# Performance work log

Hardware: AMD Instinct MI355X
Metric: run time of the kernel (lower is better)

The kernel has to match this reference:

```python
import jax, jax.numpy as jnp
import numpy as np

K = 512           # num_embeddings
D = 256           # embedding_dim
GRID = (16, 32)   # SOM grid, prod == K
SIGMA = 2.0       # Gaussian neighborhood width (blur at step 0)
COMMITMENT_COST = 0.25
KOHONEN_COST = 1.0


def _make_blur_matrix():
    # Grid.init id->coord: coord[j] = (i // prod(shape[:j])) % shape[j]
    idx = np.arange(K)
    c0 = idx % GRID[0]
    c1 = (idx // GRID[0]) % GRID[1]
    coords = np.stack([c0, c1], axis=-1).astype(np.float32)  # [K, 2]
    dist = np.linalg.norm(coords[None, :, :] - coords[:, None, :], axis=-1)  # [K, K]
    return jnp.asarray(np.exp(-(dist ** 2) / (2.0 * SIGMA ** 2)), dtype=jnp.float32)


def setup_inputs() -> dict:
    key = jax.random.key(0)
    kx, kw = jax.random.split(key)
    x = jax.random.normal(kx, (64, 32, 32, D), dtype=jnp.float32)
    w = jax.random.normal(kw, (K, D), dtype=jnp.float32)
    bmat = _make_blur_matrix()  # [K, K] constant buffer
    return {"x": x, "w": w, "bmat": bmat}


def reference(x, w, bmat):
    sg = jax.lax.stop_gradient
    flat = x.reshape(-1, D)  # [N, D]

    # nearest-code search (no_grad in torch)
    fw = sg(flat)
    ww = sg(w)
    dists = (jnp.sum(fw ** 2, axis=1, keepdims=True)
             + jnp.sum(ww ** 2, axis=1)
             - 2.0 * fw @ ww.T)                       # [N, K]
    enc_idx = jnp.argmin(dists, axis=1)               # [N]
    encodings = jax.nn.one_hot(enc_idx, K, dtype=jnp.float32)  # [N, K]

    # embedding lookup (differentiable w.r.t. w)
    quant_flat = w[enc_idx]                           # [N, D]
    quantized = quant_flat.reshape(x.shape)

    # l2_batch(w, quantized.detach()) -> [N, K]
    qd = sg(quant_flat)
    diff = (jnp.sum(w ** 2, axis=1)[None, :]
            + jnp.sum(qd ** 2, axis=1, keepdims=True)
            - 2.0 * qd @ w.T)                         # [N, K]

    # blur-weighted kohonen loss: bmm(diff[N,1,K], bmat[idx][N,K,1]).mean()
    selected = bmat[enc_idx]                          # [N, K]
    kohonen_loss = jnp.mean(jnp.sum(diff * selected, axis=-1))

    avg_probs = jnp.mean(encodings, axis=0)
    perplexity = jnp.exp(-jnp.sum(avg_probs * jnp.log(avg_probs + 1e-10)))

    e_latent = jnp.mean((sg(quantized) - x) ** 2)
    q_latent = jnp.mean((quantized - sg(x)) ** 2)
    loss = q_latent + COMMITMENT_COST * e_latent + KOHONEN_COST * kohonen_loss

    quantized_st = x + sg(quantized - x)              # straight-through
    return loss, quantized_st, perplexity, enc_idx
```

## Files before the change

### kernel.cpp

```cpp
#include <hip/hip_runtime.h>
#include <hip/hip_bf16.h>
#include <hip/hip_fp16.h>
#include <math.h>

#define NPTS 65536
#define DIM  256
#define KC   512

#define BM    128
#define NBLK  (NPTS / BM)
#define XSTR  264
#define EPS   0.01f

#define QOFF  1
#define PIDX  16777217
#define EOFF  16777218

#define XSQ_OFF   532480
#define CAND_OFF  794624
#define WS_NEEDED (CAND_OFF + (size_t)8 * 65536 * 16)

typedef _Float16 h8    __attribute__((ext_vector_type(8)));
typedef float    f32x4 __attribute__((ext_vector_type(4)));

__device__ inline void cvt_split8(float4 a, float4 b, h8& hv, h8& lv) {
    float f[8] = {a.x, a.y, a.z, a.w, b.x, b.y, b.z, b.w};
    #pragma unroll
    for (int i = 0; i < 8; ++i) {
        _Float16 h = (_Float16)f[i];
        hv[i] = h;
        lv[i] = (_Float16)(f[i] - (float)h);
    }
}

__device__ inline void merge_top2(float& b1, int& i1, float& b2, int& i2,
                                  float ob1, int oi1, float ob2, int oi2) {
    bool ow = (ob1 < b1) || (ob1 == b1 && oi1 < i1);
    float lb = ow ? b1 : ob1; int li = ow ? i1 : oi1;
    if (ow) { b1 = ob1; i1 = oi1; }
    float c2 = b2; int ci = i2;
    if (ob2 < c2 || (ob2 == c2 && oi2 < ci)) { c2 = ob2; ci = oi2; }
    if (lb  < c2 || (lb  == c2 && li  < ci)) { c2 = lb;  ci = li;  }
    b2 = c2; i2 = ci;
}

__device__ inline float exact_dist(const float* __restrict__ xr,
                                   const float* __restrict__ w, int c, float wsqc) {
    const float* wr = w + (size_t)c * DIM;
    float d0 = 0.f, d1 = 0.f, d2 = 0.f, d3 = 0.f;
    #pragma unroll 4
    for (int d = 0; d < DIM; d += 4) {
        d0 = fmaf(xr[d + 0], wr[d + 0], d0);
        d1 = fmaf(xr[d + 1], wr[d + 1], d1);
        d2 = fmaf(xr[d + 2], wr[d + 2], d2);
        d3 = fmaf(xr[d + 3], wr[d + 3], d3);
    }
    return wsqc - 2.f * ((d0 + d1) + (d2 + d3));
}

__global__ __launch_bounds__(256) void som_wsq(const float* __restrict__ w,
                                               float* __restrict__ wsq,
                                               int* __restrict__ hist,
                                               double* __restrict__ mse_acc)
{
    int k = blockIdx.x * 256 + threadIdx.x;
    const float4* r = reinterpret_cast<const float4*>(w + (size_t)k * DIM);
    float s0 = 0.f, s1 = 0.f, s2 = 0.f, s3 = 0.f;
    #pragma unroll 8
    for (int q = 0; q < DIM / 4; ++q) {
        float4 v = r[q];
        s0 = fmaf(v.x, v.x, s0);
        s1 = fmaf(v.y, v.y, s1);
        s2 = fmaf(v.z, v.z, s2);
        s3 = fmaf(v.w, v.w, s3);
    }
    wsq[k] = (s0 + s1) + (s2 + s3);
    hist[k] = 0;
    if (k == 0) *mse_acc = 0.0;
}

__global__ __launch_bounds__(256) void som_conv(const float* __restrict__ w,
                                                _Float16* __restrict__ wfh,
                                                _Float16* __restrict__ wfl)
{
    const int tid = threadIdx.x;
    const int row = blockIdx.x * 8 + (tid >> 5);
    const int g   = tid & 31;
    const float4* r = reinterpret_cast<const float4*>(w + (size_t)row * DIM);
    float4 a = r[g * 2], b = r[g * 2 + 1];
    h8 hv, lv; cvt_split8(a, b, hv, lv);
    int dsl = g >> 2, kg = g & 3;
    int ctg = row >> 4, l15 = row & 15;
    size_t off = (((size_t)(ctg * 8 + dsl)) * 4 + kg) * 128 + l15 * 8;
    *reinterpret_cast<h8*>(wfh + off) = hv;
    *reinterpret_cast<h8*>(wfl + off) = lv;
}

__global__ __launch_bounds__(1024) void som_main2(const float* __restrict__ x,
                                                  const _Float16* __restrict__ wfh,
                                                  const _Float16* __restrict__ wfl,
                                                  const float* __restrict__ wsq,
                                                  float4* __restrict__ cand,
                                                  float* __restrict__ xsq_g)
{
    alignas(16) __shared__ _Float16 xh[BM * XSTR];
    alignas(16) __shared__ _Float16 xl[BM * XSTR];
    __shared__ float wsq_s[KC];

    const int tid  = threadIdx.x;
    const int lane = tid & 63;
    const int wid  = tid >> 6;
    const int l15  = lane & 15;
    const int kg   = lane >> 4;
    const int pgrp = wid & 1;
    const int cgrp = wid >> 1;
    const int ptBlock = blockIdx.x * BM;

    const float4* xg4 = reinterpret_cast<const float4*>(x);
    #pragma unroll
    for (int it = 0; it < 4; ++it) {
        int u = it * 1024 + tid, row = u >> 5, c8 = u & 31;
        float4 a = xg4[(size_t)(ptBlock + row) * 64 + c8 * 2];
        float4 b = xg4[(size_t)(ptBlock + row) * 64 + c8 * 2 + 1];
        h8 hv, lv; cvt_split8(a, b, hv, lv);
        *reinterpret_cast<h8*>(&xh[row * XSTR + c8 * 8]) = hv;
        *reinterpret_cast<h8*>(&xl[row * XSTR + c8 * 8]) = lv;
        float s = ((fmaf(a.x, a.x, a.y * a.y) + fmaf(a.z, a.z, a.w * a.w))
                 + (fmaf(b.x, b.x, b.y * b.y) + fmaf(b.z, b.z, b.w * b.w)));
        #pragma unroll
        for (int m = 1; m <= 16; m <<= 1) s += __shfl_xor(s, m, 64);
        if ((lane & 31) == 0) xsq_g[ptBlock + row] = s;
    }
    if (tid < KC) wsq_s[tid] = wsq[tid];
    __syncthreads();

    float sb[4], ss[4];
    int   ib[4], is2[4];
    #pragma unroll
    for (int ct = 0; ct < 4; ++ct) { sb[ct] = INFINITY; ss[ct] = INFINITY; ib[ct] = 0; is2[ct] = 0; }

    #pragma unroll 1
    for (int pass = 0; pass < 2; ++pass) {
        f32x4 acc[2][4];
        #pragma unroll
        for (int rt = 0; rt < 2; ++rt)
            #pragma unroll
            for (int ct = 0; ct < 4; ++ct)
                acc[rt][ct] = (f32x4){0.f, 0.f, 0.f, 0.f};

        #pragma unroll 1
        for (int dsl = 0; dsl < 8; ++dsl) {
            int boff0 = (pgrp * 64 + l15) * XSTR + dsl * 32 + kg * 8;
            h8 Bh[4];
            #pragma unroll
            for (int ct = 0; ct < 4; ++ct)
                Bh[ct] = *reinterpret_cast<const h8*>(&xh[boff0 + ct * 16 * XSTR]);
            h8 Ah[2], Al[2];
            #pragma unroll
            for (int rt = 0; rt < 2; ++rt) {
                int ctg = pass * 16 + cgrp * 2 + rt;
                size_t aoff = ((size_t)ctg * 8 + dsl) * 512 + kg * 128 + l15 * 8;
                Ah[rt] = *reinterpret_cast<const h8*>(wfh + aoff);
                Al[rt] = *reinterpret_cast<const h8*>(wfl + aoff);
            }
            #pragma unroll
            for (int rt = 0; rt < 2; ++rt)
                #pragma unroll
                for (int ct = 0; ct < 4; ++ct)
                    acc[rt][ct] = __builtin_amdgcn_mfma_f32_16x16x32_f16(Ah[rt], Bh[ct], acc[rt][ct], 0, 0, 0);
            #pragma unroll
            for (int rt = 0; rt < 2; ++rt)
                #pragma unroll
                for (int ct = 0; ct < 4; ++ct)
                    acc[rt][ct] = __builtin_amdgcn_mfma_f32_16x16x32_f16(Al[rt], Bh[ct], acc[rt][ct], 0, 0, 0);
            h8 Bl[4];
            #pragma unroll
            for (int ct = 0; ct < 4; ++ct)
                Bl[ct] = *reinterpret_cast<const h8*>(&xl[boff0 + ct * 16 * XSTR]);
            #pragma unroll
            for (int rt = 0; rt < 2; ++rt)
                #pragma unroll
                for (int ct = 0; ct < 4; ++ct)
                    acc[rt][ct] = __builtin_amdgcn_mfma_f32_16x16x32_f16(Ah[rt], Bl[ct], acc[rt][ct], 0, 0, 0);
        }

        #pragma unroll
        for (int rt = 0; rt < 2; ++rt) {
            #pragma unroll
            for (int r = 0; r < 4; ++r) {
                int cc = pass * 256 + cgrp * 32 + rt * 16 + kg * 4 + r;
                float wq = wsq_s[cc];
                #pragma unroll
                for (int ct = 0; ct < 4; ++ct) {
                    float d = wq - 2.f * acc[rt][ct][r];
                    if (d < sb[ct] || (d == sb[ct] && cc < ib[ct])) {
                        ss[ct] = sb[ct]; is2[ct] = ib[ct]; sb[ct] = d; ib[ct] = cc;
                    } else if (d < ss[ct] || (d == ss[ct] && cc < is2[ct])) {
                        ss[ct] = d; is2[ct] = cc;
                    }
                }
            }
        }
    }

    #pragma unroll
    for (int ct = 0; ct < 4; ++ct) {
        #pragma unroll
        for (int m = 16; m <= 32; m <<= 1) {
            float ob1 = __shfl_xor(sb[ct], m, 64), ob2 = __shfl_xor(ss[ct], m, 64);
            int   oi1 = __shfl_xor(ib[ct], m, 64), oi2 = __shfl_xor(is2[ct], m, 64);
            merge_top2(sb[ct], ib[ct], ss[ct], is2[ct], ob1, oi1, ob2, oi2);
        }
    }
    if (kg == 0) {
        #pragma unroll
        for (int ct = 0; ct < 4; ++ct) {
            int p = ptBlock + pgrp * 64 + ct * 16 + l15;
            float4 v;
            v.x = sb[ct]; v.y = ss[ct];
            v.z = __int_as_float(ib[ct]); v.w = __int_as_float(is2[ct]);
            cand[(cgrp << 16) + p] = v;
        }
    }
}

__global__ __launch_bounds__(256) void som_tail(const float* __restrict__ x,
                                                const float* __restrict__ w,
                                                const float4* __restrict__ cand,
                                                const float* __restrict__ xsq_g,
                                                const float* __restrict__ wsq,
                                                float* __restrict__ out,
                                                int* __restrict__ hist,
                                                double* __restrict__ mse_acc)
{
    __shared__ float wsq_s[KC];
    __shared__ int   bidx_s[256];
    __shared__ float wsum[4];

    const int tid  = threadIdx.x;
    const int lane = tid & 63;
    const int wid  = tid >> 6;
    const int p    = blockIdx.x * 256 + tid;

    wsq_s[tid] = wsq[tid];
    wsq_s[256 + tid] = wsq[256 + tid];

    float4 c0 = cand[p];
    float b = c0.x, s = c0.y;
    int  bi = __float_as_int(c0.z), si = __float_as_int(c0.w);
    #pragma unroll
    for (int g = 1; g < 8; ++g) {
        float4 cg = cand[(g << 16) + p];
        merge_top2(b, bi, s, si, cg.x, __float_as_int(cg.z), cg.y, __float_as_int(cg.w));
    }
    __syncthreads();

    if (s - b < EPS) {
        const float* xrp = x + (size_t)p * DIM;
        float d1 = exact_dist(xrp, w, bi, wsq_s[bi]);
        float d2 = exact_dist(xrp, w, si, wsq_s[si]);
        if (d2 < d1 || (d2 == d1 && si < bi)) { bi = si; b = d2; } else { b = d1; }
    }
    bidx_s[tid] = bi;
    out[EOFF + p] = (float)bi;
    atomicAdd(&hist[bi], 1);

    float msum = xsq_g[p] + b;
    #pragma unroll
    for (int m = 32; m; m >>= 1) msum += __shfl_xor(msum, m, 64);
    if (lane == 0) wsum[wid] = msum;
    __syncthreads();
    if (tid == 0)
        atomicAdd(mse_acc, (double)((wsum[0] + wsum[1]) + (wsum[2] + wsum[3])));

    const float4* wg4 = reinterpret_cast<const float4*>(w);
    float4* q4 = reinterpret_cast<float4*>(out + QOFF);
    const size_t pBase = (size_t)blockIdx.x * 256;
    #pragma unroll 4
    for (int it = 0; it < 64; ++it) {
        int row = it * 4 + wid;
        int cc = bidx_s[row];
        q4[(pBase + row) * 64 + lane] = wg4[(size_t)cc * 64 + lane];
    }
}

__global__ __launch_bounds__(1024) void som_main_fused(const float* __restrict__ x,
                                                       const float* __restrict__ w,
                                                       const _Float16* __restrict__ wfh,
                                                       const _Float16* __restrict__ wfl,
                                                       float* __restrict__ out,
                                                       const float* __restrict__ wsq,
                                                       int* __restrict__ hist,
                                                       double* __restrict__ mse_acc)
{
    alignas(16) __shared__ _Float16 xh[BM * XSTR];
    alignas(16) __shared__ _Float16 xl[BM * XSTR];
    __shared__ float wsq_s[KC];
    __shared__ float xsq_s[BM];
    __shared__ float wsum[2];

    float* red_b  = reinterpret_cast<float*>(xh);
    float* red_s  = red_b + 8 * BM;
    int*   red_ib = reinterpret_cast<int*>(red_s + 8 * BM);
    int*   red_is = red_ib + 8 * BM;
    int*   bidx_s = reinterpret_cast<int*>(xl);

    const int tid  = threadIdx.x;
    const int lane = tid & 63;
    const int wid  = tid >> 6;
    const int l15  = lane & 15;
    const int kg   = lane >> 4;
    const int pgrp = wid & 1;
    const int cgrp = wid >> 1;
    const int ptBlock = blockIdx.x * BM;

    const float4* xg4 = reinterpret_cast<const float4*>(x);
    #pragma unroll
    for (int it = 0; it < 4; ++it) {
        int u = it * 1024 + tid, row = u >> 5, c8 = u & 31;
        float4 a = xg4[(size_t)(ptBlock + row) * 64 + c8 * 2];
        float4 b = xg4[(size_t)(ptBlock + row) * 64 + c8 * 2 + 1];
        h8 hv, lv; cvt_split8(a, b, hv, lv);
        *reinterpret_cast<h8*>(&xh[row * XSTR + c8 * 8]) = hv;
        *reinterpret_cast<h8*>(&xl[row * XSTR + c8 * 8]) = lv;
        float s = ((fmaf(a.x, a.x, a.y * a.y) + fmaf(a.z, a.z, a.w * a.w))
                 + (fmaf(b.x, b.x, b.y * b.y) + fmaf(b.z, b.z, b.w * b.w)));
        #pragma unroll
        for (int m = 1; m <= 16; m <<= 1) s += __shfl_xor(s, m, 64);
        if ((lane & 31) == 0) xsq_s[row] = s;
    }
    if (tid < KC) wsq_s[tid] = wsq[tid];
    __syncthreads();

    float sb[4], ss[4];
    int   ib[4], is2[4];
    #pragma unroll
    for (int ct = 0; ct < 4; ++ct) { sb[ct] = INFINITY; ss[ct] = INFINITY; ib[ct] = 0; is2[ct] = 0; }

    #pragma unroll 1
    for (int pass = 0; pass < 2; ++pass) {
        f32x4 acc[2][4];
        #pragma unroll
        for (int rt = 0; rt < 2; ++rt)
            #pragma unroll
            for (int ct = 0; ct < 4; ++ct)
                acc[rt][ct] = (f32x4){0.f, 0.f, 0.f, 0.f};

        #pragma unroll 1
        for (int dsl = 0; dsl < 8; ++dsl) {
            int boff0 = (pgrp * 64 + l15) * XSTR + dsl * 32 + kg * 8;
            h8 Bh[4];
            #pragma unroll
            for (int ct = 0; ct < 4; ++ct)
                Bh[ct] = *reinterpret_cast<const h8*>(&xh[boff0 + ct * 16 * XSTR]);
            h8 Ah[2], Al[2];
            #pragma unroll
            for (int rt = 0; rt < 2; ++rt) {
                int ctg = pass * 16 + cgrp * 2 + rt;
                size_t aoff = ((size_t)ctg * 8 + dsl) * 512 + kg * 128 + l15 * 8;
                Ah[rt] = *reinterpret_cast<const h8*>(wfh + aoff);
                Al[rt] = *reinterpret_cast<const h8*>(wfl + aoff);
            }
            #pragma unroll
            for (int rt = 0; rt < 2; ++rt)
                #pragma unroll
                for (int ct = 0; ct < 4; ++ct)
                    acc[rt][ct] = __builtin_amdgcn_mfma_f32_16x16x32_f16(Ah[rt], Bh[ct], acc[rt][ct], 0, 0, 0);
            #pragma unroll
            for (int rt = 0; rt < 2; ++rt)
                #pragma unroll
                for (int ct = 0; ct < 4; ++ct)
                    acc[rt][ct] = __builtin_amdgcn_mfma_f32_16x16x32_f16(Al[rt], Bh[ct], acc[rt][ct], 0, 0, 0);
            h8 Bl[4];
            #pragma unroll
            for (int ct = 0; ct < 4; ++ct)
                Bl[ct] = *reinterpret_cast<const h8*>(&xl[boff0 + ct * 16 * XSTR]);
            #pragma unroll
            for (int rt = 0; rt < 2; ++rt)
                #pragma unroll
                for (int ct = 0; ct < 4; ++ct)
                    acc[rt][ct] = __builtin_amdgcn_mfma_f32_16x16x32_f16(Ah[rt], Bl[ct], acc[rt][ct], 0, 0, 0);
        }

        #pragma unroll
        for (int rt = 0; rt < 2; ++rt) {
            #pragma unroll
            for (int r = 0; r < 4; ++r) {
                int cc = pass * 256 + cgrp * 32 + rt * 16 + kg * 4 + r;
                float wq = wsq_s[cc];
                #pragma unroll
                for (int ct = 0; ct < 4; ++ct) {
                    float d = wq - 2.f * acc[rt][ct][r];
                    if (d < sb[ct] || (d == sb[ct] && cc < ib[ct])) {
                        ss[ct] = sb[ct]; is2[ct] = ib[ct]; sb[ct] = d; ib[ct] = cc;
                    } else if (d < ss[ct] || (d == ss[ct] && cc < is2[ct])) {
                        ss[ct] = d; is2[ct] = cc;
                    }
                }
            }
        }
    }

    #pragma unroll
    for (int ct = 0; ct < 4; ++ct) {
        #pragma unroll
        for (int m = 16; m <= 32; m <<= 1) {
            float ob1 = __shfl_xor(sb[ct], m, 64), ob2 = __shfl_xor(ss[ct], m, 64);
            int   oi1 = __shfl_xor(ib[ct], m, 64), oi2 = __shfl_xor(is2[ct], m, 64);
            merge_top2(sb[ct], ib[ct], ss[ct], is2[ct], ob1, oi1, ob2, oi2);
        }
    }
    __syncthreads();

    if (kg == 0) {
        #pragma unroll
        for (int ct = 0; ct < 4; ++ct) {
            int p = pgrp * 64 + ct * 16 + l15;
            red_b[cgrp * BM + p] = sb[ct];  red_s[cgrp * BM + p] = ss[ct];
            red_ib[cgrp * BM + p] = ib[ct]; red_is[cgrp * BM + p] = is2[ct];
        }
    }
    __syncthreads();

    if (tid < BM) {
        float b = red_b[tid], s = red_s[tid];
        int  bi = red_ib[tid], si = red_is[tid];
        #pragma unroll
        for (int g = 1; g < 8; ++g)
            merge_top2(b, bi, s, si, red_b[g * BM + tid], red_ib[g * BM + tid],
                       red_s[g * BM + tid], red_is[g * BM + tid]);

        if (s - b < EPS) {
            const float* xrp = x + (size_t)(ptBlock + tid) * DIM;
            float d1 = exact_dist(xrp, w, bi, wsq_s[bi]);
            float d2 = exact_dist(xrp, w, si, wsq_s[si]);
            if (d2 < d1 || (d2 == d1 && si < bi)) { bi = si; b = d2; } else { b = d1; }
        }
        bidx_s[tid] = bi;
        out[EOFF + ptBlock + tid] = (float)bi;
        atomicAdd(&hist[bi], 1);

        float msum = xsq_s[tid] + b;
        #pragma unroll
        for (int m = 32; m; m >>= 1) msum += __shfl_xor(msum, m, 64);
        if (lane == 0) wsum[wid] = msum;
    }
    __syncthreads();
    if (tid == 0) atomicAdd(mse_acc, (double)(wsum[0] + wsum[1]));

    {
        const float4* wg4 = reinterpret_cast<const float4*>(w);
        float4* q4 = reinterpret_cast<float4*>(out + QOFF);
        #pragma unroll
        for (int r8 = 0; r8 < 8; ++r8) {
            int row = r8 * 16 + wid;
            int cc = bidx_s[row];
            q4[(size_t)(ptBlock + row) * 64 + lane] = wg4[(size_t)cc * 64 + lane];
        }
    }
}

__global__ __launch_bounds__(256) void som_g(const float* __restrict__ w,
                                             const float* __restrict__ bmat,
                                             const float* __restrict__ wsq,
                                             float* __restrict__ g)
{
    __shared__ float wj[DIM];
    __shared__ float psum[4];
    const int j = blockIdx.x;
    const int tid = threadIdx.x;
    wj[tid] = w[(size_t)j * DIM + tid];
    __syncthreads();
    const float wsqj = wsq[j];
    float sum = 0.f;
    for (int k = tid; k < KC; k += 256) {
        const float* wk = &w[(size_t)k * DIM];
        float d0 = 0.f, d1 = 0.f, d2 = 0.f, d3 = 0.f;
        #pragma unroll 4
        for (int d = 0; d < DIM; d += 4) {
            d0 = fmaf(wj[d + 0], wk[d + 0], d0);
            d1 = fmaf(wj[d + 1], wk[d + 1], d1);
            d2 = fmaf(wj[d + 2], wk[d + 2], d2);
            d3 = fmaf(wj[d + 3], wk[d + 3], d3);
        }
        float dot = (d0 + d1) + (d2 + d3);
        float t = wsq[k] + wsqj - 2.f * dot;
        sum = fmaf(bmat[(size_t)j * KC + k], t, sum);
    }
    #pragma unroll
    for (int m = 32; m; m >>= 1) sum += __shfl_xor(sum, m, 64);
    int lane = tid & 63, wid = tid >> 6;
    if (lane == 0) psum[wid] = sum;
    __syncthreads();
    if (tid == 0) g[j] = (psum[0] + psum[1]) + (psum[2] + psum[3]);
}

__global__ __launch_bounds__(512) void som_final(const int* __restrict__ hist,
                                                 const float* __restrict__ g,
                                                 const double* __restrict__ mse_acc,
                                                 float* __restrict__ out)
{
    __shared__ float e_part[8], k_part[8];
    const int tid = threadIdx.x;
    int cnt = hist[tid];
    float p = (float)cnt / (float)NPTS;
    float ent = -p * logf(p + 1e-10f);
    float koh = (float)cnt * g[tid];
    #pragma unroll
    for (int m = 32; m; m >>= 1) {
        ent += __shfl_xor(ent, m, 64);
        koh += __shfl_xor(koh, m, 64);
    }
    int lane = tid & 63, wid = tid >> 6;
    if (lane == 0) { e_part[wid] = ent; k_part[wid] = koh; }
    __syncthreads();
    if (tid == 0) {
        float es = 0.f, ks = 0.f;
        #pragma unroll
        for (int i = 0; i < 8; ++i) { es += e_part[i]; ks += k_part[i]; }
        float mse = (float)(*mse_acc / (double)(NPTS * (size_t)DIM));
        out[0] = fmaf(1.25f, mse, ks / (float)NPTS);
        out[PIDX] = expf(es);
    }
}

extern "C" void kernel_launch(void* const* d_in, const int* in_sizes, int n_in,
                              void* d_out, int out_size, void* d_ws, size_t ws_size,
                              hipStream_t stream) {
    const float* x    = (const float*)d_in[0];
    const float* w    = (const float*)d_in[1];
    const float* bmat = (const float*)d_in[2];
    float* out = (float*)d_out;

    _Float16* wfh = (_Float16*)d_ws;
    _Float16* wfl = wfh + 131072;
    float*  wsq  = (float*)((char*)d_ws + 524288);
    float*  g    = (float*)((char*)d_ws + 526336);
    int*    hist = (int*)((char*)d_ws + 528384);
    double* mse  = (double*)((char*)d_ws + 530432);

    som_wsq  <<<2, 256, 0, stream>>>(w, wsq, hist, mse);
    som_conv <<<64, 256, 0, stream>>>(w, wfh, wfl);

    if (ws_size >= WS_NEEDED) {
        float*  xsq_g = (float*)((char*)d_ws + XSQ_OFF);
        float4* cand  = (float4*)((char*)d_ws + CAND_OFF);
        som_main2<<<NBLK, 1024, 0, stream>>>(x, wfh, wfl, wsq, cand, xsq_g);
        som_tail <<<256, 256, 0, stream>>>(x, w, cand, xsq_g, wsq, out, hist, mse);
    } else {
        som_main_fused<<<NBLK, 1024, 0, stream>>>(x, w, wfh, wfl, out, wsq, hist, mse);
    }

    som_g    <<<KC, 256, 0, stream>>>(w, bmat, wsq, g);
    som_final<<<1, KC, 0, stream>>>(hist, g, mse, out);
}
```

Baseline: 180.2 us.

## Split tail kernel into many small 16-point blocks for candidate merge and gather

The tail kernel used to run 256 blocks of 256 points each and copy 256 codebook rows per block. It now runs 4096 blocks of 16 points: 128 threads stage the candidate records in shared memory, 16 threads merge them and do the exact-distance refinement, and all four waves copy 16 rows. This spreads the gather and the global-memory latency over many more blocks so the GPU stays busy. In exchange it issues 16 times more MSE double atomics, and most threads sit idle during the merge phase.

```diff
diff --git a/kernel.cpp b/kernel.cpp
--- a/kernel.cpp
+++ b/kernel.cpp
@@ -224,63 +224,63 @@
     }
 }
 
-__global__ __launch_bounds__(256) void som_tail(const float* __restrict__ x,
-                                                const float* __restrict__ w,
-                                                const float4* __restrict__ cand,
-                                                const float* __restrict__ xsq_g,
-                                                const float* __restrict__ wsq,
-                                                float* __restrict__ out,
-                                                int* __restrict__ hist,
-                                                double* __restrict__ mse_acc)
-{
-    __shared__ float wsq_s[KC];
-    __shared__ int   bidx_s[256];
-    __shared__ float wsum[4];
+__global__ __launch_bounds__(256) void som_quant2(const float* __restrict__ x,
+                                                  const float* __restrict__ w,
+                                                  const float4* __restrict__ cand,
+                                                  const float* __restrict__ xsq_g,
+                                                  const float* __restrict__ wsq,
+                                                  float* __restrict__ out,
+                                                  int* __restrict__ hist,
+                                                  double* __restrict__ mse_acc)
+{
+    __shared__ float4 cl[8][16];
+    __shared__ int    bidx_s[16];
 
     const int tid  = threadIdx.x;
     const int lane = tid & 63;
     const int wid  = tid >> 6;
-    const int p    = blockIdx.x * 256 + tid;
-
-    wsq_s[tid] = wsq[tid];
-    wsq_s[256 + tid] = wsq[256 + tid];
-
-    float4 c0 = cand[p];
-    float b = c0.x, s = c0.y;
-    int  bi = __float_as_int(c0.z), si = __float_as_int(c0.w);
-    #pragma unroll
-    for (int g = 1; g < 8; ++g) {
-        float4 cg = cand[(g << 16) + p];
-        merge_top2(b, bi, s, si, cg.x, __float_as_int(cg.z), cg.y, __float_as_int(cg.w));
-    }
-    __syncthreads();
-
-    if (s - b < EPS) {
-        const float* xrp = x + (size_t)p * DIM;
-        float d1 = exact_dist(xrp, w, bi, wsq_s[bi]);
-        float d2 = exact_dist(xrp, w, si, wsq_s[si]);
-        if (d2 < d1 || (d2 == d1 && si < bi)) { bi = si; b = d2; } else { b = d1; }
-    }
-    bidx_s[tid] = bi;
-    out[EOFF + p] = (float)bi;
-    atomicAdd(&hist[bi], 1);
-
-    float msum = xsq_g[p] + b;
-    #pragma unroll
-    for (int m = 32; m; m >>= 1) msum += __shfl_xor(msum, m, 64);
-    if (lane == 0) wsum[wid] = msum;
-    __syncthreads();
-    if (tid == 0)
-        atomicAdd(mse_acc, (double)((wsum[0] + wsum[1]) + (wsum[2] + wsum[3])));
+    const int pBase = blockIdx.x << 4;
+
+    if (tid < 128) {
+        int g = tid >> 4, i = tid & 15;
+        cl[g][i] = cand[(g << 16) + pBase + i];
+    }
+    __syncthreads();
+
+    if (tid < 16) {
+        const int p = pBase + tid;
+        float4 c0 = cl[0][tid];
+        float b = c0.x, s = c0.y;
+        int  bi = __float_as_int(c0.z), si = __float_as_int(c0.w);
+        #pragma unroll
+        for (int g = 1; g < 8; ++g) {
+            float4 cg = cl[g][tid];
+            merge_top2(b, bi, s, si, cg.x, __float_as_int(cg.z), cg.y, __float_as_int(cg.w));
+        }
+        if (s - b < EPS) {
+            const float* xrp = x + (size_t)p * DIM;
+            float d1 = exact_dist(xrp, w, bi, wsq[bi]);
+            float d2 = exact_dist(xrp, w, si, wsq[si]);
+            if (d2 < d1 || (d2 == d1 && si < bi)) { bi = si; b = d2; } else { b = d1; }
+        }
+        bidx_s[tid] = bi;
+        out[EOFF + p] = (float)bi;
+        atomicAdd(&hist[bi], 1);
+
+        float ms = xsq_g[p] + b;
+        #pragma unroll
+        for (int m = 1; m <= 8; m <<= 1) ms += __shfl_xor(ms, m, 64);
+        if (tid == 0) atomicAdd(mse_acc, (double)ms);
+    }
+    __syncthreads();
 
     const float4* wg4 = reinterpret_cast<const float4*>(w);
     float4* q4 = reinterpret_cast<float4*>(out + QOFF);
-    const size_t pBase = (size_t)blockIdx.x * 256;
-    #pragma unroll 4
-    for (int it = 0; it < 64; ++it) {
+    #pragma unroll
+    for (int it = 0; it < 4; ++it) {
         int row = it * 4 + wid;
         int cc = bidx_s[row];
-        q4[(pBase + row) * 64 + lane] = wg4[(size_t)cc * 64 + lane];
+        q4[((size_t)pBase + row) * 64 + lane] = wg4[(size_t)cc * 64 + lane];
     }
 }
 
@@ -545,8 +545,8 @@
     if (ws_size >= WS_NEEDED) {
         float*  xsq_g = (float*)((char*)d_ws + XSQ_OFF);
         float4* cand  = (float4*)((char*)d_ws + CAND_OFF);
-        som_main2<<<NBLK, 1024, 0, stream>>>(x, wfh, wfl, wsq, cand, xsq_g);
-        som_tail <<<256, 256, 0, stream>>>(x, w, cand, xsq_g, wsq, out, hist, mse);
+        som_main2 <<<NBLK, 1024, 0, stream>>>(x, wfh, wfl, wsq, cand, xsq_g);
+        som_quant2<<<NPTS / 16, 256, 0, stream>>>(x, w, cand, xsq_g, wsq, out, hist, mse);
     } else {
         som_main_fused<<<NBLK, 1024, 0, stream>>>(x, w, wfh, wfl, out, wsq, hist, mse);
     }
```

Result: slower. 188.8 us (+4.8%).
